# Performance work log

Hardware: AMD Instinct MI355X
Metric: run time of the kernel (lower is better)

## Reference

```python
import jax, jax.numpy as jnp
from jax import lax
import numpy as np

B, S, D = 32, 2048, 512

def setup_inputs() -> dict:
    key = jax.random.key(0)
    ks = jax.random.split(key, 9)
    inv = 1.0 / np.sqrt(D).astype(np.float32)
    return {
        "query": jax.random.normal(ks[0], (B, 1, D), jnp.float32),
        "value": jax.random.normal(ks[1], (B, S, D), jnp.float32),
        "last_alignment_energy": jax.random.uniform(ks[2], (B, S), jnp.float32),
        "conv_w": jax.random.normal(ks[3], (D, 1, 3), jnp.float32) * 0.1,  # Conv1d(1->D,k=3)
        "conv_b": jax.random.normal(ks[4], (D,), jnp.float32) * 0.01,
        "w_q": jax.random.normal(ks[5], (D, D), jnp.float32) * inv,  # applied as x @ w_q
        "w_v": jax.random.normal(ks[6], (D, D), jnp.float32) * inv,
        "bias": jax.random.uniform(ks[7], (D,), jnp.float32, minval=-0.1, maxval=0.1),
        "score_w": jax.random.normal(ks[8], (D,), jnp.float32) * inv,  # score_proj weight (out=1)
        "score_b": jnp.zeros((), jnp.float32),
    }


def reference(query, value, last_alignment_energy, conv_w, conv_b, w_q, w_v, bias, score_w, score_b):
    # location features: Conv1d(1->D, k=3, pad=1) over the previous alignment
    loc = lax.conv_general_dilated(
        last_alignment_energy[:, None, :], conv_w,
        window_strides=(1,), padding=[(1, 1)],
        dimension_numbers=("NCH", "OIH", "NCH"))  # [B, D, S]
    loc = jnp.transpose(loc, (0, 2, 1)) + conv_b  # [B, S, D]

    # additive attention energy: tanh(Wq q + Wv v + loc + b) @ score_w
    hidden = jnp.tanh(query @ w_q + value @ w_v + loc + bias)  # [B, S, D] (query broadcasts over S)
    scores = hidden @ score_w + score_b                          # [B, S]
    align = jax.nn.softmax(scores, axis=-1)                      # [B, S]

    # context = align^T V
    context = jnp.einsum("bs,bsd->bd", align, value)             # [B, D]
    return context, align
```

## Files before the change

### kernel.cpp

```cpp
#include <hip/hip_runtime.h>
#include <hip/hip_bf16.h>

#define B_ 32
#define S_ 2048
#define D_ 512
#define M_ (B_*S_)

typedef __bf16 bf16x8 __attribute__((ext_vector_type(8)));
typedef float  f32x4  __attribute__((ext_vector_type(4)));

__device__ __forceinline__ float tanh_fast(float x){
  float e2 = __expf(2.f * x);
  return 1.f - 2.f * __builtin_amdgcn_rcpf(e2 + 1.f);
}

__device__ __forceinline__ bf16x8 pack8(f32x4 r0, f32x4 r1){
  bf16x8 t;
  t[0]=(__bf16)r0[0]; t[1]=(__bf16)r0[1]; t[2]=(__bf16)r0[2]; t[3]=(__bf16)r0[3];
  t[4]=(__bf16)r1[0]; t[5]=(__bf16)r1[1]; t[6]=(__bf16)r1[2]; t[7]=(__bf16)r1[3];
  return t;
}

__device__ __forceinline__ void gl_lds16(const float* g, float* l){
  __builtin_amdgcn_global_load_lds(
      (const __attribute__((address_space(1))) void*)g,
      (__attribute__((address_space(3))) void*)l, 16, 0, 0);
}

__global__ void k_reorder_wv(const float* __restrict__ wv,
                             unsigned short* __restrict__ wvr){
  int frag = blockIdx.x;
  int lane = threadIdx.x;
  int ks = frag >> 5, nt = frag & 31;
  int k0 = ks*32 + (lane>>4)*8;
  int d  = nt*16 + (lane&15);
  bf16x8 t;
  #pragma unroll
  for (int j=0;j<8;++j) t[j] = (__bf16)wv[(k0+j)*D_ + d];
  *reinterpret_cast<uint4*>(wvr + ((size_t)frag*64 + lane)*8) =
      __builtin_bit_cast(uint4, t);
}

__global__ void k_qproj(const float* __restrict__ q,
                        const float* __restrict__ wq,
                        const float* __restrict__ bias,
                        float* __restrict__ qp){
  int b  = blockIdx.y;
  int t  = threadIdx.x;
  int dl = t & 127, eg = t >> 7;
  int d  = blockIdx.x*128 + dl;
  __shared__ float qs[D_];
  __shared__ float red[4][128];
  for (int e=t; e<D_; e+=512) qs[e] = q[b*D_+e];
  __syncthreads();
  float acc = 0.f;
  #pragma unroll 8
  for (int i=0;i<128;++i){
    int e = eg*128 + i;
    acc = fmaf(qs[e], wq[(size_t)e*D_+d], acc);
  }
  red[eg][dl] = acc;
  __syncthreads();
  if (eg == 0)
    qp[b*D_+d] = red[0][dl]+red[1][dl]+red[2][dl]+red[3][dl] + bias[d];
}

__launch_bounds__(256, 2)
__global__ void k_energy(const float* __restrict__ value,
                         const unsigned short* __restrict__ wvr,
                         const float* __restrict__ qp,
                         const float* __restrict__ energy,
                         const float* __restrict__ conv_w,
                         const float* __restrict__ conv_b,
                         const float* __restrict__ score_w,
                         float* __restrict__ scores){
  const int t    = threadIdx.x;
  const int wave = t >> 6;
  const int lane = t & 63;
  const int quad = lane >> 4;
  const int lm   = lane & 15;
  const int row0 = blockIdx.x * 64;
  const int b    = row0 >> 11;
  const int s0   = row0 & (S_-1);

  __shared__ __align__(16) float Af[2][4096];

  int soff[4];
  #pragma unroll
  for (int i=0;i<4;++i){
    int rq  = 4*i + quad;
    int f   = ((rq&7)<<1) | (rq>>3);
    soff[i] = (row0 + wave*16 + rq)*D_ + ((lm ^ f)<<2);
  }

  const int fl  = ((lm&7)<<1) | (lm>>3);
  const int p00 = (quad*2)     ^ fl;
  const int p01 = (quad*2 + 1) ^ fl;

  f32x4 acc[4][8];
  #pragma unroll
  for (int mt=0;mt<4;++mt)
    #pragma unroll
    for (int nt=0;nt<8;++nt)
      acc[mt][nt] = (f32x4){0.f,0.f,0.f,0.f};

  const unsigned short* bP = wvr + ((size_t)(wave*8)*64 + lane)*8;

  #pragma unroll
  for (int i=0;i<4;++i)
    gl_lds16(value + soff[i], &Af[0][(wave*4+i)*256]);
  bf16x8 b0[8], b1[8];
  #pragma unroll
  for (int n=0;n<8;++n)
    b0[n] = __builtin_bit_cast(bf16x8,
        *reinterpret_cast<const uint4*>(bP + (size_t)n*512));
  __syncthreads();

  for (int p=0; p<8; ++p){
    const int buf = p & 1;

    if (p < 7){
      #pragma unroll
      for (int i=0;i<4;++i)
        gl_lds16(value + soff[i] + (p+1)*64, &Af[buf^1][(wave*4+i)*256]);
    }

    #pragma unroll
    for (int n=0;n<8;++n)
      b1[n] = __builtin_bit_cast(bf16x8,
          *reinterpret_cast<const uint4*>(bP + (size_t)((2*p+1)*32+n)*512));

    bf16x8 a[4];
    #pragma unroll
    for (int mt=0;mt<4;++mt){
      const float* base = &Af[buf][(mt*16+lm)*64];
      f32x4 r0 = *reinterpret_cast<const f32x4*>(base + (p00<<2));
      f32x4 r1 = *reinterpret_cast<const f32x4*>(base + (p01<<2));
      a[mt] = pack8(r0, r1);
    }
    __builtin_amdgcn_s_setprio(1);
    #pragma unroll
    for (int ntl=0;ntl<8;++ntl)
      #pragma unroll
      for (int mt=0;mt<4;++mt)
        acc[mt][ntl] = __builtin_amdgcn_mfma_f32_16x16x32_bf16(a[mt], b0[ntl], acc[mt][ntl], 0,0,0);
    __builtin_amdgcn_s_setprio(0);

    if (p < 7){
      #pragma unroll
      for (int n=0;n<8;++n)
        b0[n] = __builtin_bit_cast(bf16x8,
            *reinterpret_cast<const uint4*>(bP + (size_t)((2*p+2)*32+n)*512));
    }

    #pragma unroll
    for (int mt=0;mt<4;++mt){
      const float* base = &Af[buf][(mt*16+lm)*64];
      f32x4 r0 = *reinterpret_cast<const f32x4*>(base + ((p00^8)<<2));
      f32x4 r1 = *reinterpret_cast<const f32x4*>(base + ((p01^8)<<2));
      a[mt] = pack8(r0, r1);
    }
    __builtin_amdgcn_s_setprio(1);
    #pragma unroll
    for (int ntl=0;ntl<8;++ntl)
      #pragma unroll
      for (int mt=0;mt<4;++mt)
        acc[mt][ntl] = __builtin_amdgcn_mfma_f32_16x16x32_bf16(a[mt], b1[ntl], acc[mt][ntl], 0,0,0);
    __builtin_amdgcn_s_setprio(0);

    __syncthreads();
  }

  float sw[8], c0[8], c1[8], c2[8], cb[8], qv[8];
  #pragma unroll
  for (int ntl=0; ntl<8; ++ntl){
    int d = wave*128 + ntl*16 + lm;
    sw[ntl] = score_w[d];
    c0[ntl] = conv_w[d*3+0];
    c1[ntl] = conv_w[d*3+1];
    c2[ntl] = conv_w[d*3+2];
    cb[ntl] = conv_b[d];
    qv[ntl] = qp[b*D_+d];
  }
  float* red = &Af[0][0];
  const float* eB = energy + b*S_;
  #pragma unroll
  for (int mt=0; mt<4; ++mt){
    #pragma unroll
    for (int r=0;r<4;++r){
      int sl = mt*16 + quad*4 + r;
      int s  = s0 + sl;
      float em1 = (s > 0)    ? eB[s-1] : 0.f;
      float e0  =              eB[s];
      float ep1 = (s < S_-1) ? eB[s+1] : 0.f;
      float p = 0.f;
      #pragma unroll
      for (int ntl=0; ntl<8; ++ntl){
        float h = acc[mt][ntl][r] + qv[ntl]
                + fmaf(c0[ntl],em1, fmaf(c1[ntl],e0, fmaf(c2[ntl],ep1, cb[ntl])));
        p = fmaf(sw[ntl], tanh_fast(h), p);
      }
      #pragma unroll
      for (int m=1; m<16; m<<=1) p += __shfl_xor(p, m, 64);
      if (lm == 0) red[wave*64 + sl] = p;
    }
  }
  __syncthreads();
  if (t < 64)
    scores[row0 + t] = red[t] + red[64+t] + red[128+t] + red[192+t];
}

__global__ void k_softmax(const float* __restrict__ sp,
                          const float* __restrict__ score_b,
                          float* __restrict__ out_align){
  int b = blockIdx.x, t = threadIdx.x;
  int lane = t & 63, wid = t >> 6;
  float sb = score_b[0];
  float v[8], mx = -3.4e38f;
  #pragma unroll
  for (int i=0;i<8;++i){
    float sc = sp[b*S_ + t + i*256] + sb;
    v[i] = sc;
    mx = fmaxf(mx, sc);
  }
  __shared__ float red[4], red2[4];
  #pragma unroll
  for (int m=1;m<64;m<<=1) mx = fmaxf(mx, __shfl_xor(mx, m, 64));
  if (lane==0) red[wid] = mx;
  __syncthreads();
  mx = fmaxf(fmaxf(red[0],red[1]), fmaxf(red[2],red[3]));
  float sum = 0.f;
  #pragma unroll
  for (int i=0;i<8;++i){ v[i] = __expf(v[i]-mx); sum += v[i]; }
  #pragma unroll
  for (int m=1;m<64;m<<=1) sum += __shfl_xor(sum, m, 64);
  if (lane==0) red2[wid] = sum;
  __syncthreads();
  sum = red2[0]+red2[1]+red2[2]+red2[3];
  float inv = 1.f/sum;
  #pragma unroll
  for (int i=0;i<8;++i) out_align[b*S_ + t + i*256] = v[i]*inv;
}

__global__ void k_ctx_part(const float* __restrict__ value,
                           const float* __restrict__ align,
                           float* __restrict__ cpart){
  int b = blockIdx.y, sc = blockIdx.x;
  int t = threadIdx.x;
  int r = t >> 7;
  int c = (t & 127) * 4;
  __shared__ float al[64];
  if (t < 64) al[t] = align[b*S_ + sc*64 + t];
  __syncthreads();
  f32x4 acc = (f32x4){0.f,0.f,0.f,0.f};
  const float* vbase = value + ((size_t)(b*S_ + sc*64 + r))*D_ + c;
  #pragma unroll 8
  for (int i=0;i<32;++i){
    f32x4 v = *reinterpret_cast<const f32x4*>(vbase + (size_t)(2*i)*D_);
    acc += al[2*i+r] * v;
  }
  __shared__ float lred[2][D_];
  #pragma unroll
  for (int j=0;j<4;++j) lred[r][c+j] = acc[j];
  __syncthreads();
  if (r == 0){
    #pragma unroll
    for (int j=0;j<4;++j)
      cpart[((size_t)(b*32+sc))*D_ + c + j] = lred[0][c+j] + lred[1][c+j];
  }
}

__global__ void k_ctx_reduce(const float* __restrict__ cpart,
                             float* __restrict__ out_ctx){
  int idx = blockIdx.x*256 + threadIdx.x;
  int b = idx >> 9, d = idx & 511;
  float s = 0.f;
  #pragma unroll
  for (int j=0;j<32;++j) s += cpart[((size_t)(b*32+j))*D_ + d];
  out_ctx[idx] = s;
}

extern "C" void kernel_launch(void* const* d_in, const int* in_sizes, int n_in,
                              void* d_out, int out_size, void* d_ws, size_t ws_size,
                              hipStream_t stream){
  const float* query   = (const float*)d_in[0];
  const float* value   = (const float*)d_in[1];
  const float* energy  = (const float*)d_in[2];
  const float* conv_w  = (const float*)d_in[3];
  const float* conv_b  = (const float*)d_in[4];
  const float* w_q     = (const float*)d_in[5];
  const float* w_v     = (const float*)d_in[6];
  const float* bias    = (const float*)d_in[7];
  const float* score_w = (const float*)d_in[8];
  const float* score_b = (const float*)d_in[9];

  char* ws = (char*)d_ws;
  unsigned short* wvr = (unsigned short*)(ws);
  float* qp    = (float*)(ws + (512<<10));
  float* sp    = (float*)(ws + (576<<10));
  float* cpart = (float*)(ws + (832<<10));

  float* out_ctx   = (float*)d_out;
  float* out_align = out_ctx + B_*D_;

  k_reorder_wv<<<dim3(512),      dim3(64),  0, stream>>>(w_v, wvr);
  k_qproj     <<<dim3(4,32),     dim3(512), 0, stream>>>(query, w_q, bias, qp);
  k_energy    <<<dim3(M_/64),    dim3(256), 0, stream>>>(value, wvr, qp, energy,
                                                         conv_w, conv_b, score_w, sp);
  k_softmax   <<<dim3(B_),       dim3(256), 0, stream>>>(sp, score_b, out_align);
  k_ctx_part  <<<dim3(32,B_),    dim3(256), 0, stream>>>(value, out_align, cpart);
  k_ctx_reduce<<<dim3(B_*D_/256),dim3(256), 0, stream>>>(cpart, out_ctx);
}
```

Measured before the change: 269.8 us.

## Shrink energy tile to 32 rows with full-K LDS load, merge prep kernels, atomic ctx

The energy kernel now loads a whole 32x512 value tile into LDS up front, instead of double-buffering 64-row K-chunks with a barrier per step. This halves the accumulator count per wave and doubles the number of blocks. The W_v reorder and query projection are merged into one prep kernel. The context reduction kernel is replaced by atomicAdd into an output that the softmax kernel zeroes. Together these cut launch count and per-step synchronisation, at the cost of 64KB LDS per block (which may limit occupancy), no overlap of loads with MFMA, and reloading W_v fragments twice as often in total.

Result: slower. 293.5 us (+8.8%).

```diff
diff --git a/kernel.cpp b/kernel.cpp
--- a/kernel.cpp
+++ b/kernel.cpp
@@ -27,42 +27,43 @@
       (__attribute__((address_space(3))) void*)l, 16, 0, 0);
 }
 
-__global__ void k_reorder_wv(const float* __restrict__ wv,
-                             unsigned short* __restrict__ wvr){
-  int frag = blockIdx.x;
-  int lane = threadIdx.x;
-  int ks = frag >> 5, nt = frag & 31;
-  int k0 = ks*32 + (lane>>4)*8;
-  int d  = nt*16 + (lane&15);
-  bf16x8 t;
-  #pragma unroll
-  for (int j=0;j<8;++j) t[j] = (__bf16)wv[(k0+j)*D_ + d];
-  *reinterpret_cast<uint4*>(wvr + ((size_t)frag*64 + lane)*8) =
-      __builtin_bit_cast(uint4, t);
-}
-
-__global__ void k_qproj(const float* __restrict__ q,
-                        const float* __restrict__ wq,
-                        const float* __restrict__ bias,
-                        float* __restrict__ qp){
-  int b  = blockIdx.y;
-  int t  = threadIdx.x;
-  int dl = t & 127, eg = t >> 7;
-  int d  = blockIdx.x*128 + dl;
+__global__ void k_prep(const float* __restrict__ wv,
+                       unsigned short* __restrict__ wvr,
+                       const float* __restrict__ q,
+                       const float* __restrict__ wq,
+                       const float* __restrict__ bias,
+                       float* __restrict__ qp){
   __shared__ float qs[D_];
-  __shared__ float red[4][128];
-  for (int e=t; e<D_; e+=512) qs[e] = q[b*D_+e];
-  __syncthreads();
-  float acc = 0.f;
-  #pragma unroll 8
-  for (int i=0;i<128;++i){
-    int e = eg*128 + i;
-    acc = fmaf(qs[e], wq[(size_t)e*D_+d], acc);
-  }
-  red[eg][dl] = acc;
-  __syncthreads();
-  if (eg == 0)
-    qp[b*D_+d] = red[0][dl]+red[1][dl]+red[2][dl]+red[3][dl] + bias[d];
+  __shared__ float red2[2][128];
+  int bid = blockIdx.x, t = threadIdx.x;
+  if (bid < 128){
+    int frag = bid*4 + (t>>6);
+    int lane = t & 63;
+    int ks = frag >> 5, nt = frag & 31;
+    int k0 = ks*32 + (lane>>4)*8;
+    int d  = nt*16 + (lane&15);
+    bf16x8 v;
+    #pragma unroll
+    for (int j=0;j<8;++j) v[j] = (__bf16)wv[(k0+j)*D_ + d];
+    *reinterpret_cast<uint4*>(wvr + ((size_t)frag*64 + lane)*8) =
+        __builtin_bit_cast(uint4, v);
+  } else {
+    int idx = bid - 128;
+    int b = idx >> 2, ch = idx & 3;
+    int dl = t & 127, eg = t >> 7;
+    int d  = ch*128 + dl;
+    for (int e=t; e<D_; e+=256) qs[e] = q[b*D_+e];
+    __syncthreads();
+    float a = 0.f;
+    #pragma unroll 8
+    for (int i=0;i<256;++i){
+      int e = eg*256 + i;
+      a = fmaf(qs[e], wq[(size_t)e*D_+d], a);
+    }
+    red2[eg][dl] = a;
+    __syncthreads();
+    if (eg == 0) qp[b*D_+d] = red2[0][dl] + red2[1][dl] + bias[d];
+  }
 }
 
 __launch_bounds__(256, 2)
@@ -79,113 +80,77 @@
   const int lane = t & 63;
   const int quad = lane >> 4;
   const int lm   = lane & 15;
-  const int row0 = blockIdx.x * 64;
+  const int row0 = blockIdx.x * 32;
   const int b    = row0 >> 11;
   const int s0   = row0 & (S_-1);
 
-  __shared__ __align__(16) float Af[2][4096];
-
-  int soff[4];
-  #pragma unroll
-  for (int i=0;i<4;++i){
-    int rq  = 4*i + quad;
-    int f   = ((rq&7)<<1) | (rq>>3);
-    soff[i] = (row0 + wave*16 + rq)*D_ + ((lm ^ f)<<2);
-  }
-
-  const int fl  = ((lm&7)<<1) | (lm>>3);
-  const int p00 = (quad*2)     ^ fl;
-  const int p01 = (quad*2 + 1) ^ fl;
-
-  f32x4 acc[4][8];
-  #pragma unroll
-  for (int mt=0;mt<4;++mt)
-    #pragma unroll
-    for (int nt=0;nt<8;++nt)
-      acc[mt][nt] = (f32x4){0.f,0.f,0.f,0.f};
+  __shared__ __align__(16) float Af[32*512];
+
+  #pragma unroll
+  for (int i=0;i<16;++i){
+    int j  = wave*16 + i;
+    int r  = j >> 1;
+    int x  = ((r&7)<<1) | ((r>>3)&1);
+    int pg = ((j&1)<<6) | lane;
+    gl_lds16(value + (size_t)(row0+r)*D_ + ((pg ^ x)<<2), &Af[j*256]);
+  }
+
+  f32x4 acc[2][8];
+  #pragma unroll
+  for (int mt=0;mt<2;++mt)
+    #pragma unroll
+    for (int n=0;n<8;++n)
+      acc[mt][n] = (f32x4){0.f,0.f,0.f,0.f};
 
   const unsigned short* bP = wvr + ((size_t)(wave*8)*64 + lane)*8;
-
-  #pragma unroll
-  for (int i=0;i<4;++i)
-    gl_lds16(value + soff[i], &Af[0][(wave*4+i)*256]);
-  bf16x8 b0[8], b1[8];
+  bf16x8 bc[8];
   #pragma unroll
   for (int n=0;n<8;++n)
-    b0[n] = __builtin_bit_cast(bf16x8,
+    bc[n] = __builtin_bit_cast(bf16x8,
         *reinterpret_cast<const uint4*>(bP + (size_t)n*512));
-  __syncthreads();
-
-  for (int p=0; p<8; ++p){
-    const int buf = p & 1;
-
-    if (p < 7){
-      #pragma unroll
-      for (int i=0;i<4;++i)
-        gl_lds16(value + soff[i] + (p+1)*64, &Af[buf^1][(wave*4+i)*256]);
-    }
-
-    #pragma unroll
-    for (int n=0;n<8;++n)
-      b1[n] = __builtin_bit_cast(bf16x8,
-          *reinterpret_cast<const uint4*>(bP + (size_t)((2*p+1)*32+n)*512));
-
-    bf16x8 a[4];
-    #pragma unroll
-    for (int mt=0;mt<4;++mt){
-      const float* base = &Af[buf][(mt*16+lm)*64];
-      f32x4 r0 = *reinterpret_cast<const f32x4*>(base + (p00<<2));
-      f32x4 r1 = *reinterpret_cast<const f32x4*>(base + (p01<<2));
+
+  __syncthreads();
+
+  const int fl = ((lm&7)<<1) | (lm>>3);
+  for (int c=0;c<16;++c){
+    bf16x8 a[2];
+    #pragma unroll
+    for (int mt=0;mt<2;++mt){
+      const float* base = &Af[(mt*16+lm)*512];
+      int ga = (c*8 + quad*2) ^ fl;
+      f32x4 r0 = *reinterpret_cast<const f32x4*>(base + ga*4);
+      f32x4 r1 = *reinterpret_cast<const f32x4*>(base + (ga^1)*4);
       a[mt] = pack8(r0, r1);
     }
     __builtin_amdgcn_s_setprio(1);
     #pragma unroll
-    for (int ntl=0;ntl<8;++ntl)
-      #pragma unroll
-      for (int mt=0;mt<4;++mt)
-        acc[mt][ntl] = __builtin_amdgcn_mfma_f32_16x16x32_bf16(a[mt], b0[ntl], acc[mt][ntl], 0,0,0);
+    for (int n=0;n<8;++n){
+      bf16x8 bv = bc[n];
+      if (c < 15)
+        bc[n] = __builtin_bit_cast(bf16x8,
+            *reinterpret_cast<const uint4*>(bP + (size_t)((c+1)*32+n)*512));
+      acc[0][n] = __builtin_amdgcn_mfma_f32_16x16x32_bf16(a[0], bv, acc[0][n], 0,0,0);
+      acc[1][n] = __builtin_amdgcn_mfma_f32_16x16x32_bf16(a[1], bv, acc[1][n], 0,0,0);
+    }
     __builtin_amdgcn_s_setprio(0);
-
-    if (p < 7){
-      #pragma unroll
-      for (int n=0;n<8;++n)
-        b0[n] = __builtin_bit_cast(bf16x8,
-            *reinterpret_cast<const uint4*>(bP + (size_t)((2*p+2)*32+n)*512));
-    }
-
-    #pragma unroll
-    for (int mt=0;mt<4;++mt){
-      const float* base = &Af[buf][(mt*16+lm)*64];
-      f32x4 r0 = *reinterpret_cast<const f32x4*>(base + ((p00^8)<<2));
-      f32x4 r1 = *reinterpret_cast<const f32x4*>(base + ((p01^8)<<2));
-      a[mt] = pack8(r0, r1);
-    }
-    __builtin_amdgcn_s_setprio(1);
-    #pragma unroll
-    for (int ntl=0;ntl<8;++ntl)
-      #pragma unroll
-      for (int mt=0;mt<4;++mt)
-        acc[mt][ntl] = __builtin_amdgcn_mfma_f32_16x16x32_bf16(a[mt], b1[ntl], acc[mt][ntl], 0,0,0);
-    __builtin_amdgcn_s_setprio(0);
-
-    __syncthreads();
   }
 
   float sw[8], c0[8], c1[8], c2[8], cb[8], qv[8];
   #pragma unroll
-  for (int ntl=0; ntl<8; ++ntl){
-    int d = wave*128 + ntl*16 + lm;
-    sw[ntl] = score_w[d];
-    c0[ntl] = conv_w[d*3+0];
-    c1[ntl] = conv_w[d*3+1];
-    c2[ntl] = conv_w[d*3+2];
-    cb[ntl] = conv_b[d];
-    qv[ntl] = qp[b*D_+d];
-  }
-  float* red = &Af[0][0];
+  for (int n=0; n<8; ++n){
+    int d = wave*128 + n*16 + lm;
+    sw[n] = score_w[d];
+    c0[n] = conv_w[d*3+0];
+    c1[n] = conv_w[d*3+1];
+    c2[n] = conv_w[d*3+2];
+    cb[n] = conv_b[d];
+    qv[n] = qp[b*D_+d];
+  }
+  __syncthreads();
+  float* red = &Af[0];
   const float* eB = energy + b*S_;
   #pragma unroll
-  for (int mt=0; mt<4; ++mt){
+  for (int mt=0; mt<2; ++mt){
     #pragma unroll
     for (int r=0;r<4;++r){
       int sl = mt*16 + quad*4 + r;
@@ -195,26 +160,29 @@
       float ep1 = (s < S_-1) ? eB[s+1] : 0.f;
       float p = 0.f;
       #pragma unroll
-      for (int ntl=0; ntl<8; ++ntl){
-        float h = acc[mt][ntl][r] + qv[ntl]
-                + fmaf(c0[ntl],em1, fmaf(c1[ntl],e0, fmaf(c2[ntl],ep1, cb[ntl])));
-        p = fmaf(sw[ntl], tanh_fast(h), p);
+      for (int n=0; n<8; ++n){
+        float h = acc[mt][n][r] + qv[n]
+                + fmaf(c0[n],em1, fmaf(c1[n],e0, fmaf(c2[n],ep1, cb[n])));
+        p = fmaf(sw[n], tanh_fast(h), p);
       }
       #pragma unroll
       for (int m=1; m<16; m<<=1) p += __shfl_xor(p, m, 64);
-      if (lm == 0) red[wave*64 + sl] = p;
-    }
-  }
-  __syncthreads();
-  if (t < 64)
-    scores[row0 + t] = red[t] + red[64+t] + red[128+t] + red[192+t];
+      if (lm == 0) red[wave*32 + sl] = p;
+    }
+  }
+  __syncthreads();
+  if (t < 32)
+    scores[row0 + t] = red[t] + red[32+t] + red[64+t] + red[96+t];
 }
 
 __global__ void k_softmax(const float* __restrict__ sp,
                           const float* __restrict__ score_b,
-                          float* __restrict__ out_align){
+                          float* __restrict__ out_align,
+                          float* __restrict__ out_ctx){
   int b = blockIdx.x, t = threadIdx.x;
   int lane = t & 63, wid = t >> 6;
+  out_ctx[b*D_ + t]       = 0.f;
+  out_ctx[b*D_ + 256 + t] = 0.f;
   float sb = score_b[0];
   float v[8], mx = -3.4e38f;
   #pragma unroll
@@ -244,7 +212,7 @@
 
 __global__ void k_ctx_part(const float* __restrict__ value,
                            const float* __restrict__ align,
-                           float* __restrict__ cpart){
+                           float* __restrict__ out_ctx){
   int b = blockIdx.y, sc = blockIdx.x;
   int t = threadIdx.x;
   int r = t >> 7;
@@ -266,18 +234,8 @@
   if (r == 0){
     #pragma unroll
     for (int j=0;j<4;++j)
-      cpart[((size_t)(b*32+sc))*D_ + c + j] = lred[0][c+j] + lred[1][c+j];
-  }
-}
-
-__global__ void k_ctx_reduce(const float* __restrict__ cpart,
-                             float* __restrict__ out_ctx){
-  int idx = blockIdx.x*256 + threadIdx.x;
-  int b = idx >> 9, d = idx & 511;
-  float s = 0.f;
-  #pragma unroll
-  for (int j=0;j<32;++j) s += cpart[((size_t)(b*32+j))*D_ + d];
-  out_ctx[idx] = s;
+      atomicAdd(&out_ctx[(size_t)b*D_ + c + j], lred[0][c+j] + lred[1][c+j]);
+  }
 }
 
 extern "C" void kernel_launch(void* const* d_in, const int* in_sizes, int n_in,
@@ -298,16 +256,13 @@
   unsigned short* wvr = (unsigned short*)(ws);
   float* qp    = (float*)(ws + (512<<10));
   float* sp    = (float*)(ws + (576<<10));
-  float* cpart = (float*)(ws + (832<<10));
 
   float* out_ctx   = (float*)d_out;
   float* out_align = out_ctx + B_*D_;
 
-  k_reorder_wv<<<dim3(512),      dim3(64),  0, stream>>>(w_v, wvr);
-  k_qproj     <<<dim3(4,32),     dim3(512), 0, stream>>>(query, w_q, bias, qp);
-  k_energy    <<<dim3(M_/64),    dim3(256), 0, stream>>>(value, wvr, qp, energy,
-                                                         conv_w, conv_b, score_w, sp);
-  k_softmax   <<<dim3(B_),       dim3(256), 0, stream>>>(sp, score_b, out_align);
-  k_ctx_part  <<<dim3(32,B_),    dim3(256), 0, stream>>>(value, out_align, cpart);
-  k_ctx_reduce<<<dim3(B_*D_/256),dim3(256), 0, stream>>>(cpart, out_ctx);
-}
+  k_prep    <<<dim3(256),     dim3(256), 0, stream>>>(w_v, wvr, query, w_q, bias, qp);
+  k_energy  <<<dim3(M_/32),   dim3(256), 0, stream>>>(value, wvr, qp, energy,
+                                                      conv_w, conv_b, score_w, sp);
+  k_softmax <<<dim3(B_),      dim3(256), 0, stream>>>(sp, score_b, out_align, out_ctx);
+  k_ctx_part<<<dim3(32,B_),   dim3(256), 0, stream>>>(value, out_align, out_ctx);
+}
```
